# Performance work log

Measured on AMD Instinct MI355X. Metric: run time of the kernel, lower is better.

## Reference

```python
import jax, jax.numpy as jnp
import numpy as np

D = 1024      # in_features
E = 8         # num_experts
H = 4 * D     # expert hidden (expert_hidden_scale=4)
B, S = 2, 2048


def setup_inputs() -> dict:
    key = jax.random.key(0)
    k0, k1, k2, k3 = jax.random.split(key, 4)
    scale = 0.02
    x = jax.random.normal(k0, (B, S, D), dtype=jnp.float32)
    W_gate = (jax.random.normal(k1, (D, E), dtype=jnp.float32) * scale)      # gate.weight.T
    fc1_w = (jax.random.normal(k2, (E, 2 * H, D), dtype=jnp.float32) * scale)  # per-expert fc1 [out=2H, in=D]
    fc1_b = jnp.zeros((E, 2 * H), dtype=jnp.float32)
    fc2_w = (jax.random.normal(k3, (E, D, H), dtype=jnp.float32) * scale)      # per-expert fc2 [out=D, in=H]
    fc2_b = jnp.zeros((E, D), dtype=jnp.float32)
    return {"x": x, "W_gate": W_gate, "fc1_w": fc1_w, "fc1_b": fc1_b,
            "fc2_w": fc2_w, "fc2_b": fc2_b, "top_k": 2}


def reference(x, W_gate, fc1_w, fc1_b, fc2_w, fc2_b, top_k):
    # x: [B, S, D]. Dropout is identity (eval mode).
    b, s, d = x.shape
    e = W_gate.shape[1]
    xf = x.reshape(-1, d)                      # [N, D]
    n = xf.shape[0]

    gate_logits = xf @ W_gate                  # [N, E]
    top_vals, top_idx = jax.lax.top_k(gate_logits, top_k)          # [N, K]
    top_w = jax.nn.softmax(top_vals.astype(jnp.float32), axis=-1).astype(x.dtype)  # [N, K]

    # Every expert processes every token (matches the dense one-hot dispatch:
    # masked-out tokens get zero combine weight, so results are identical).
    h = jnp.einsum('nd,ehd->enh', xf, fc1_w) + fc1_b[:, None, :]   # [E, N, 2H]
    gate_h, val_h = jnp.split(h, 2, axis=-1)
    act = jax.nn.silu(gate_h) * val_h                               # [E, N, H]
    expert_out = jnp.einsum('enh,edh->end', act, fc2_w) + fc2_b[:, None, :]  # [E, N, D]

    onehot = jax.nn.one_hot(top_idx, e, dtype=x.dtype)             # [N, K, E]
    combine = jnp.einsum('nke,nk->en', onehot, top_w)              # [E, N]
    y = jnp.einsum('end,en->nd', expert_out, combine).reshape(b, s, d)

    frac_per_expert = onehot.sum(axis=(0, 1)) / n                  # [E]
    mean_prob = jax.nn.softmax(gate_logits, axis=-1).mean(axis=0)  # [E]
    aux_loss = e * jnp.sum(frac_per_expert * mean_prob)
    return y, aux_loss
```

## Files before the change

### kernel.cpp

```cpp
#include <hip/hip_runtime.h>
#include <hip/hip_bf16.h>
#include <cstdint>

#define NTOK 4096
#define DIM 1024
#define NEXP 8
#define HID 4096
#define TWO_H 8192
#define RCAP (NTOK*NEXP)
#define TOTROWS (NTOK*2)
#define ROWPAD (TOTROWS + 128)

typedef __attribute__((ext_vector_type(8))) short short8;
typedef __attribute__((ext_vector_type(4))) float f32x4;

__device__ __forceinline__ void async16(const void* g, void* l) {
    __builtin_amdgcn_global_load_lds(
        (const __attribute__((address_space(1))) unsigned int*)g,
        (__attribute__((address_space(3))) unsigned int*)l, 16, 0, 0);
}

__device__ __forceinline__ unsigned int packbf2(float a, float b) {
    union { __hip_bfloat16 h[2]; unsigned int u; } t;
    t.h[0] = __float2bfloat16(a); t.h[1] = __float2bfloat16(b);
    return t.u;
}

__global__ __launch_bounds__(256) void convert_kernel(const float* __restrict__ src,
                                                      __hip_bfloat16* __restrict__ dst, int n8) {
    int i = blockIdx.x * 256 + threadIdx.x;
    if (i >= n8) return;
    const float4* s = (const float4*)src + (size_t)i * 2;
    float4 a = s[0], b = s[1];
    uint4 o;
    o.x = packbf2(a.x, a.y); o.y = packbf2(a.z, a.w);
    o.z = packbf2(b.x, b.y); o.w = packbf2(b.z, b.w);
    ((uint4*)dst)[i] = o;
}

__global__ __launch_bounds__(256) void gate_kernel(
    const float* __restrict__ x, const float* __restrict__ Wg,
    float* __restrict__ p, float* __restrict__ topw,
    int* __restrict__ tok_list, int* __restrict__ klist, int* __restrict__ counts) {
    int n = blockIdx.x * 4 + (threadIdx.x >> 6);
    int lane = threadIdx.x & 63;
    const float* xr = x + (size_t)n * DIM;
    float acc[8];
#pragma unroll
    for (int e = 0; e < 8; e++) acc[e] = 0.f;
#pragma unroll
    for (int i = 0; i < 16; i++) {
        int d = i * 64 + lane;
        float xv = xr[d];
        const float4* wrow = (const float4*)(Wg + (size_t)d * 8);
        float4 w0 = wrow[0], w1 = wrow[1];
        acc[0] += xv * w0.x; acc[1] += xv * w0.y; acc[2] += xv * w0.z; acc[3] += xv * w0.w;
        acc[4] += xv * w1.x; acc[5] += xv * w1.y; acc[6] += xv * w1.z; acc[7] += xv * w1.w;
    }
#pragma unroll
    for (int m = 1; m < 64; m <<= 1) {
#pragma unroll
        for (int e = 0; e < 8; e++) acc[e] += __shfl_xor(acc[e], m, 64);
    }
    if (lane == 0) {
        int i0 = 0; float v0 = acc[0];
#pragma unroll
        for (int e = 1; e < 8; e++) if (acc[e] > v0) { v0 = acc[e]; i0 = e; }
        int i1 = -1; float v1 = -1e30f;
#pragma unroll
        for (int e = 0; e < 8; e++) if (e != i0 && acc[e] > v1) { v1 = acc[e]; i1 = e; }
        float ee = __expf(v1 - v0);
        float s = 1.f + ee;
        topw[2 * n] = 1.f / s;
        topw[2 * n + 1] = ee / s;
        float se = 0.f; float pe[8];
#pragma unroll
        for (int e = 0; e < 8; e++) { pe[e] = __expf(acc[e] - v0); se += pe[e]; }
        float inv = 1.f / se;
#pragma unroll
        for (int e = 0; e < 8; e++) p[(size_t)n * 8 + e] = pe[e] * inv;
        int p0 = atomicAdd(&counts[i0], 1);
        tok_list[i0 * NTOK + p0] = n; klist[i0 * NTOK + p0] = 0;
        int p1 = atomicAdd(&counts[i1], 1);
        tok_list[i1 * NTOK + p1] = n; klist[i1 * NTOK + p1] = 1;
    }
}

__global__ __launch_bounds__(256) void finalize_kernel(const float* __restrict__ p,
                                                       const int* __restrict__ counts,
                                                       int* __restrict__ offsets,
                                                       float* __restrict__ aux_out) {
    __shared__ float red[256];
    int t = threadIdx.x;
    float a = 0.f;
    for (int i = t; i < NTOK * NEXP; i += 256) a += p[i];
    red[t] = a;
    __syncthreads();
    if (t < 8) {
        float s = 0.f;
        for (int j = t; j < 256; j += 8) s += red[j];
        red[t] = s;
    }
    __syncthreads();
    if (t == 0) {
        int off = 0; float aux = 0.f;
        for (int e = 0; e < 8; e++) {
            offsets[e] = off;
            aux += ((float)counts[e] / (float)NTOK) * (red[e] / (float)NTOK);
            off += counts[e];
        }
        offsets[8] = off;
        aux_out[0] = 8.f * aux;
    }
}

__global__ __launch_bounds__(256) void pack_kernel(const float* __restrict__ x,
                                                   const int* __restrict__ tok_list,
                                                   const int* __restrict__ klist,
                                                   const int* __restrict__ counts,
                                                   const int* __restrict__ offsets,
                                                   __hip_bfloat16* __restrict__ xg,
                                                   int* __restrict__ prow) {
    int ci = blockIdx.x * 4 + (threadIdx.x >> 6);
    int lane = threadIdx.x & 63;
    int e = ci >> 12, pos = ci & (NTOK - 1);
    if (pos >= counts[e]) return;
    int tok = tok_list[ci];
    int r = offsets[e] + pos;
    const float4* src = (const float4*)(x + (size_t)tok * DIM);
    uint2* dst = (uint2*)(xg + (size_t)r * DIM);
#pragma unroll
    for (int i = 0; i < 4; i++) {
        int idx = i * 64 + lane;
        float4 v = src[idx];
        uint2 o; o.x = packbf2(v.x, v.y); o.y = packbf2(v.z, v.w);
        dst[idx] = o;
    }
    if (lane == 0) prow[tok * 2 + klist[ci]] = r;
}

__global__ __launch_bounds__(256, 2) void fc1_kernel(
    const __hip_bfloat16* __restrict__ xg, const __hip_bfloat16* __restrict__ w1b,
    const float* __restrict__ fc1b,
    __hip_bfloat16* __restrict__ act,
    const int* __restrict__ counts, const int* __restrict__ offsets) {
    int e = blockIdx.z;
    int cnt = counts[e];
    int rt = blockIdx.y;
    if (rt * 128 >= cnt) return;
    int ct = blockIdx.x;
    int row0 = offsets[e] + rt * 128;

    __shared__ __hip_bfloat16 As[128 * 64];
    __shared__ __hip_bfloat16 Bg[128 * 64];
    __shared__ __hip_bfloat16 Bv[128 * 64];

    int tid = threadIdx.x;
    int lane = tid & 63;
    int w = tid >> 6;
    int wr = w >> 1, wc = w & 1;
    int r = lane & 15, q = lane >> 4;

    const __hip_bfloat16* Abase = xg + (size_t)row0 * DIM;
    const __hip_bfloat16* Gbase = w1b + ((size_t)e * TWO_H + (size_t)ct * 128) * DIM;
    const __hip_bfloat16* Vbase = Gbase + (size_t)HID * DIM;

    size_t offA[4]; int ldsOff[4];
#pragma unroll
    for (int i = 0; i < 4; i++) {
        int c = w * 256 + i * 64 + lane;
        int m = c >> 3, kc = (c & 7) ^ (m & 7);
        offA[i] = (size_t)m * DIM + kc * 8;
        ldsOff[i] = (w * 256 + i * 64) * 8;
    }

    f32x4 accg[4][4], accv[4][4];
#pragma unroll
    for (int a = 0; a < 4; a++)
#pragma unroll
        for (int b = 0; b < 4; b++)
#pragma unroll
            for (int k = 0; k < 4; k++) { accg[a][b][k] = 0.f; accv[a][b][k] = 0.f; }

    for (int kb = 0; kb < DIM / 64; ++kb) {
        size_t ko = (size_t)kb * 64;
#pragma unroll
        for (int i = 0; i < 4; i++) {
            async16(Abase + offA[i] + ko, (void*)(As + ldsOff[i]));
            async16(Gbase + offA[i] + ko, (void*)(Bg + ldsOff[i]));
            async16(Vbase + offA[i] + ko, (void*)(Bv + ldsOff[i]));
        }
        __syncthreads();
#pragma unroll
        for (int ks = 0; ks < 2; ks++) {
            short8 af[4], bg[4], bv[4];
            int swz = ((ks * 4 + q) ^ (lane & 7)) * 8;
#pragma unroll
            for (int ti = 0; ti < 4; ti++) {
                int m = wr * 64 + ti * 16 + r;
                af[ti] = *(const short8*)(As + m * 64 + swz);
            }
#pragma unroll
            for (int tj = 0; tj < 4; tj++) {
                int n = wc * 64 + tj * 16 + r;
                bg[tj] = *(const short8*)(Bg + n * 64 + swz);
                bv[tj] = *(const short8*)(Bv + n * 64 + swz);
            }
#pragma unroll
            for (int ti = 0; ti < 4; ti++)
#pragma unroll
                for (int tj = 0; tj < 4; tj++) {
                    accg[ti][tj] = __builtin_amdgcn_mfma_f32_16x16x32_bf16(af[ti], bg[tj], accg[ti][tj], 0, 0, 0);
                    accv[ti][tj] = __builtin_amdgcn_mfma_f32_16x16x32_bf16(af[ti], bv[tj], accv[ti][tj], 0, 0, 0);
                }
        }
        __syncthreads();
    }

    const float* bgate = fc1b + (size_t)e * TWO_H + (size_t)ct * 128;
    const float* bval = bgate + HID;
#pragma unroll
    for (int ti = 0; ti < 4; ti++) {
#pragma unroll
        for (int tj = 0; tj < 4; tj++) {
            int coln = wc * 64 + tj * 16 + r;
            float bg_ = bgate[coln];
            float bv_ = bval[coln];
            f32x4 g = accg[ti][tj], v = accv[ti][tj];
#pragma unroll
            for (int rg = 0; rg < 4; rg++) {
                int lrow = wr * 64 + ti * 16 + q * 4 + rg;
                if (rt * 128 + lrow < cnt) {
                    float gv = g[rg] + bg_;
                    float vv = v[rg] + bv_;
                    float sil = gv / (1.f + __expf(-gv));
                    act[(size_t)(row0 + lrow) * HID + (size_t)ct * 128 + coln] = __float2bfloat16(sil * vv);
                }
            }
        }
    }
}

__global__ __launch_bounds__(256, 2) void fc2_kernel(
    const __hip_bfloat16* __restrict__ act, const __hip_bfloat16* __restrict__ w2b,
    const float* __restrict__ fc2b,
    float* __restrict__ eout,
    const int* __restrict__ counts, const int* __restrict__ offsets) {
    int e = blockIdx.z;
    int cnt = counts[e];
    int rt = blockIdx.y;
    if (rt * 128 >= cnt) return;
    int ct = blockIdx.x;
    int row0 = offsets[e] + rt * 128;

    __shared__ __hip_bfloat16 As[128 * 64];
    __shared__ __hip_bfloat16 Bs[128 * 64];

    int tid = threadIdx.x;
    int lane = tid & 63;
    int w = tid >> 6;
    int wr = w >> 1, wc = w & 1;
    int r = lane & 15, q = lane >> 4;

    const __hip_bfloat16* Abase = act + (size_t)row0 * HID;
    const __hip_bfloat16* Bbase = w2b + ((size_t)e * DIM + (size_t)ct * 128) * HID;

    size_t offA[4]; int ldsOff[4];
#pragma unroll
    for (int i = 0; i < 4; i++) {
        int c = w * 256 + i * 64 + lane;
        int m = c >> 3, kc = (c & 7) ^ (m & 7);
        offA[i] = (size_t)m * HID + kc * 8;
        ldsOff[i] = (w * 256 + i * 64) * 8;
    }

    f32x4 acc[4][4];
#pragma unroll
    for (int a = 0; a < 4; a++)
#pragma unroll
        for (int b = 0; b < 4; b++)
#pragma unroll
            for (int k = 0; k < 4; k++) acc[a][b][k] = 0.f;

    for (int kb = 0; kb < HID / 64; ++kb) {
        size_t ko = (size_t)kb * 64;
#pragma unroll
        for (int i = 0; i < 4; i++) {
            async16(Abase + offA[i] + ko, (void*)(As + ldsOff[i]));
            async16(Bbase + offA[i] + ko, (void*)(Bs + ldsOff[i]));
        }
        __syncthreads();
#pragma unroll
        for (int ks = 0; ks < 2; ks++) {
            short8 af[4], bf[4];
            int swz = ((ks * 4 + q) ^ (lane & 7)) * 8;
#pragma unroll
            for (int ti = 0; ti < 4; ti++) {
                int m = wr * 64 + ti * 16 + r;
                af[ti] = *(const short8*)(As + m * 64 + swz);
            }
#pragma unroll
            for (int tj = 0; tj < 4; tj++) {
                int n = wc * 64 + tj * 16 + r;
                bf[tj] = *(const short8*)(Bs + n * 64 + swz);
            }
#pragma unroll
            for (int ti = 0; ti < 4; ti++)
#pragma unroll
                for (int tj = 0; tj < 4; tj++)
                    acc[ti][tj] = __builtin_amdgcn_mfma_f32_16x16x32_bf16(af[ti], bf[tj], acc[ti][tj], 0, 0, 0);
        }
        __syncthreads();
    }

    const float* bias = fc2b + (size_t)e * DIM + (size_t)ct * 128;
#pragma unroll
    for (int ti = 0; ti < 4; ti++) {
#pragma unroll
        for (int tj = 0; tj < 4; tj++) {
            int coln = wc * 64 + tj * 16 + r;
            float b_ = bias[coln];
            f32x4 a = acc[ti][tj];
#pragma unroll
            for (int rg = 0; rg < 4; rg++) {
                int lrow = wr * 64 + ti * 16 + q * 4 + rg;
                if (rt * 128 + lrow < cnt)
                    eout[(size_t)(row0 + lrow) * DIM + (size_t)ct * 128 + coln] = a[rg] + b_;
            }
        }
    }
}

__global__ __launch_bounds__(256) void combine_kernel(const float* __restrict__ eout,
                                                      const int* __restrict__ prow,
                                                      const float* __restrict__ topw,
                                                      float* __restrict__ y) {
    int n = blockIdx.x;
    int t = threadIdx.x;
    int r0 = prow[2 * n], r1 = prow[2 * n + 1];
    float w0 = topw[2 * n], w1 = topw[2 * n + 1];
    const float4* a = (const float4*)(eout + (size_t)r0 * DIM);
    const float4* b = (const float4*)(eout + (size_t)r1 * DIM);
    float4 va = a[t], vb = b[t];
    float4 o;
    o.x = w0 * va.x + w1 * vb.x;
    o.y = w0 * va.y + w1 * vb.y;
    o.z = w0 * va.z + w1 * vb.z;
    o.w = w0 * va.w + w1 * vb.w;
    ((float4*)(y + (size_t)n * DIM))[t] = o;
}

extern "C" void kernel_launch(void* const* d_in, const int* in_sizes, int n_in,
                              void* d_out, int out_size, void* d_ws, size_t ws_size,
                              hipStream_t stream) {
    (void)in_sizes; (void)n_in; (void)out_size; (void)ws_size;
    const float* x = (const float*)d_in[0];
    const float* Wg = (const float*)d_in[1];
    const float* fc1w = (const float*)d_in[2];
    const float* fc1b = (const float*)d_in[3];
    const float* fc2w = (const float*)d_in[4];
    const float* fc2b = (const float*)d_in[5];
    float* out = (float*)d_out;

    char* wsp = (char*)d_ws;
    __hip_bfloat16* w1b = (__hip_bfloat16*)wsp;  wsp += (size_t)NEXP * TWO_H * DIM * 2;
    __hip_bfloat16* w2b = (__hip_bfloat16*)wsp;  wsp += (size_t)NEXP * DIM * HID * 2;
    __hip_bfloat16* xg = (__hip_bfloat16*)wsp;   wsp += (size_t)ROWPAD * DIM * 2;
    __hip_bfloat16* act = (__hip_bfloat16*)wsp;  wsp += (size_t)ROWPAD * HID * 2;
    float* eout = (float*)wsp;                   wsp += (size_t)TOTROWS * DIM * 4;
    float* p = (float*)wsp;                      wsp += (size_t)NTOK * NEXP * 4;
    float* topw = (float*)wsp;                   wsp += (size_t)NTOK * 2 * 4;
    int* tok_list = (int*)wsp;                   wsp += (size_t)RCAP * 4;
    int* klist = (int*)wsp;                      wsp += (size_t)RCAP * 4;
    int* prow = (int*)wsp;                       wsp += (size_t)NTOK * 2 * 4;
    int* counts = (int*)wsp;                     wsp += 64;
    int* offsets = (int*)wsp;                    wsp += 64;

    hipMemsetAsync(counts, 0, 8 * sizeof(int), stream);
    convert_kernel<<<32768, 256, 0, stream>>>(fc1w, w1b, (int)(NEXP * TWO_H * DIM / 8));
    convert_kernel<<<16384, 256, 0, stream>>>(fc2w, w2b, (int)(NEXP * DIM * HID / 8));
    gate_kernel<<<NTOK / 4, 256, 0, stream>>>(x, Wg, p, topw, tok_list, klist, counts);
    finalize_kernel<<<1, 256, 0, stream>>>(p, counts, offsets, out + (size_t)NTOK * DIM);
    pack_kernel<<<RCAP / 4, 256, 0, stream>>>(x, tok_list, klist, counts, offsets, xg, prow);
    fc1_kernel<<<dim3(HID / 128, 32, NEXP), 256, 0, stream>>>(xg, w1b, fc1b, act, counts, offsets);
    fc2_kernel<<<dim3(DIM / 128, 32, NEXP), 256, 0, stream>>>(act, w2b, fc2b, eout, counts, offsets);
    combine_kernel<<<NTOK, 256, 0, stream>>>(eout, prow, topw, out);
}
```

Baseline: 972.0 us.

## Fuse fp32-to-bf16 weight conversion into MoE GEMM B-operand loads

Removes the two standalone kernels that converted the full fc1 and fc2 weight tensors to bf16 in workspace. Each GEMM now reads fp32 weights straight from global memory into registers and packs them into bf16 MFMA fragments, skipping LDS for the B operand. Warp tiling changes so each wave covers all 128 rows and 32 columns, reusing the B fragments across 8 A fragments read from LDS. This drops a large conversion pass and its bf16 writes. In exchange, fp32 weights are re-read by every row tile at twice the bytes, and the global loads are not prefetched, so their latency is exposed before each barrier.

```diff
diff --git a/kernel.cpp b/kernel.cpp
--- a/kernel.cpp
+++ b/kernel.cpp
@@ -26,16 +26,11 @@
     return t.u;
 }
 
-__global__ __launch_bounds__(256) void convert_kernel(const float* __restrict__ src,
-                                                      __hip_bfloat16* __restrict__ dst, int n8) {
-    int i = blockIdx.x * 256 + threadIdx.x;
-    if (i >= n8) return;
-    const float4* s = (const float4*)src + (size_t)i * 2;
-    float4 a = s[0], b = s[1];
-    uint4 o;
-    o.x = packbf2(a.x, a.y); o.y = packbf2(a.z, a.w);
-    o.z = packbf2(b.x, b.y); o.w = packbf2(b.z, b.w);
-    ((uint4*)dst)[i] = o;
+__device__ __forceinline__ short8 cvtfrag(float4 f0, float4 f1) {
+    union { unsigned int u[4]; short8 s; } t;
+    t.u[0] = packbf2(f0.x, f0.y); t.u[1] = packbf2(f0.z, f0.w);
+    t.u[2] = packbf2(f1.x, f1.y); t.u[3] = packbf2(f1.z, f1.w);
+    return t.s;
 }
 
 __global__ __launch_bounds__(256) void gate_kernel(
@@ -140,7 +135,7 @@
 }
 
 __global__ __launch_bounds__(256, 2) void fc1_kernel(
-    const __hip_bfloat16* __restrict__ xg, const __hip_bfloat16* __restrict__ w1b,
+    const __hip_bfloat16* __restrict__ xg, const float* __restrict__ fc1w,
     const float* __restrict__ fc1b,
     __hip_bfloat16* __restrict__ act,
     const int* __restrict__ counts, const int* __restrict__ offsets) {
@@ -152,89 +147,87 @@
     int row0 = offsets[e] + rt * 128;
 
     __shared__ __hip_bfloat16 As[128 * 64];
-    __shared__ __hip_bfloat16 Bg[128 * 64];
-    __shared__ __hip_bfloat16 Bv[128 * 64];
 
     int tid = threadIdx.x;
     int lane = tid & 63;
     int w = tid >> 6;
-    int wr = w >> 1, wc = w & 1;
     int r = lane & 15, q = lane >> 4;
 
     const __hip_bfloat16* Abase = xg + (size_t)row0 * DIM;
-    const __hip_bfloat16* Gbase = w1b + ((size_t)e * TWO_H + (size_t)ct * 128) * DIM;
-    const __hip_bfloat16* Vbase = Gbase + (size_t)HID * DIM;
-
-    size_t offA[4]; int ldsOff[4];
+    const float* Gbase = fc1w + ((size_t)e * TWO_H + (size_t)ct * 128) * DIM;
+    const float* Vbase = Gbase + (size_t)HID * DIM;
+
+    size_t offA[4]; int ldsA[4];
 #pragma unroll
     for (int i = 0; i < 4; i++) {
         int c = w * 256 + i * 64 + lane;
         int m = c >> 3, kc = (c & 7) ^ (m & 7);
         offA[i] = (size_t)m * DIM + kc * 8;
-        ldsOff[i] = (w * 256 + i * 64) * 8;
-    }
-
-    f32x4 accg[4][4], accv[4][4];
-#pragma unroll
-    for (int a = 0; a < 4; a++)
-#pragma unroll
-        for (int b = 0; b < 4; b++)
+        ldsA[i] = (w * 256 + i * 64) * 8;
+    }
+
+    const float* g0 = Gbase + (size_t)(w * 32 + r) * DIM;
+    const float* g1 = Gbase + (size_t)(w * 32 + 16 + r) * DIM;
+    const float* v0 = Vbase + (size_t)(w * 32 + r) * DIM;
+    const float* v1 = Vbase + (size_t)(w * 32 + 16 + r) * DIM;
+
+    f32x4 accg[8][2], accv[8][2];
+#pragma unroll
+    for (int a = 0; a < 8; a++)
+#pragma unroll
+        for (int b = 0; b < 2; b++)
 #pragma unroll
             for (int k = 0; k < 4; k++) { accg[a][b][k] = 0.f; accv[a][b][k] = 0.f; }
 
     for (int kb = 0; kb < DIM / 64; ++kb) {
-        size_t ko = (size_t)kb * 64;
-#pragma unroll
-        for (int i = 0; i < 4; i++) {
-            async16(Abase + offA[i] + ko, (void*)(As + ldsOff[i]));
-            async16(Gbase + offA[i] + ko, (void*)(Bg + ldsOff[i]));
-            async16(Vbase + offA[i] + ko, (void*)(Bv + ldsOff[i]));
+        int ko = kb * 64;
+#pragma unroll
+        for (int i = 0; i < 4; i++) async16(Abase + offA[i] + ko, (void*)(As + ldsA[i]));
+
+        short8 bg[2][2], bv[2][2];
+#pragma unroll
+        for (int ks = 0; ks < 2; ks++) {
+            int kk = ko + ks * 32 + q * 8;
+            const float4* pg0 = (const float4*)(g0 + kk);
+            const float4* pg1 = (const float4*)(g1 + kk);
+            const float4* pv0 = (const float4*)(v0 + kk);
+            const float4* pv1 = (const float4*)(v1 + kk);
+            bg[ks][0] = cvtfrag(pg0[0], pg0[1]);
+            bg[ks][1] = cvtfrag(pg1[0], pg1[1]);
+            bv[ks][0] = cvtfrag(pv0[0], pv0[1]);
+            bv[ks][1] = cvtfrag(pv1[0], pv1[1]);
         }
         __syncthreads();
 #pragma unroll
         for (int ks = 0; ks < 2; ks++) {
-            short8 af[4], bg[4], bv[4];
             int swz = ((ks * 4 + q) ^ (lane & 7)) * 8;
 #pragma unroll
-            for (int ti = 0; ti < 4; ti++) {
-                int m = wr * 64 + ti * 16 + r;
-                af[ti] = *(const short8*)(As + m * 64 + swz);
+            for (int ti = 0; ti < 8; ti++) {
+                short8 af = *(const short8*)(As + (ti * 16 + r) * 64 + swz);
+                accg[ti][0] = __builtin_amdgcn_mfma_f32_16x16x32_bf16(af, bg[ks][0], accg[ti][0], 0, 0, 0);
+                accg[ti][1] = __builtin_amdgcn_mfma_f32_16x16x32_bf16(af, bg[ks][1], accg[ti][1], 0, 0, 0);
+                accv[ti][0] = __builtin_amdgcn_mfma_f32_16x16x32_bf16(af, bv[ks][0], accv[ti][0], 0, 0, 0);
+                accv[ti][1] = __builtin_amdgcn_mfma_f32_16x16x32_bf16(af, bv[ks][1], accv[ti][1], 0, 0, 0);
             }
-#pragma unroll
-            for (int tj = 0; tj < 4; tj++) {
-                int n = wc * 64 + tj * 16 + r;
-                bg[tj] = *(const short8*)(Bg + n * 64 + swz);
-                bv[tj] = *(const short8*)(Bv + n * 64 + swz);
-            }
-#pragma unroll
-            for (int ti = 0; ti < 4; ti++)
-#pragma unroll
-                for (int tj = 0; tj < 4; tj++) {
-                    accg[ti][tj] = __builtin_amdgcn_mfma_f32_16x16x32_bf16(af[ti], bg[tj], accg[ti][tj], 0, 0, 0);
-                    accv[ti][tj] = __builtin_amdgcn_mfma_f32_16x16x32_bf16(af[ti], bv[tj], accv[ti][tj], 0, 0, 0);
-                }
         }
         __syncthreads();
     }
 
-    const float* bgate = fc1b + (size_t)e * TWO_H + (size_t)ct * 128;
-    const float* bval = bgate + HID;
-#pragma unroll
-    for (int ti = 0; ti < 4; ti++) {
-#pragma unroll
-        for (int tj = 0; tj < 4; tj++) {
-            int coln = wc * 64 + tj * 16 + r;
-            float bg_ = bgate[coln];
-            float bv_ = bval[coln];
-            f32x4 g = accg[ti][tj], v = accv[ti][tj];
+#pragma unroll
+    for (int tj = 0; tj < 2; tj++) {
+        int cg = ct * 128 + w * 32 + tj * 16 + r;
+        float bg_ = fc1b[(size_t)e * TWO_H + cg];
+        float bv_ = fc1b[(size_t)e * TWO_H + HID + cg];
+#pragma unroll
+        for (int ti = 0; ti < 8; ti++) {
 #pragma unroll
             for (int rg = 0; rg < 4; rg++) {
-                int lrow = wr * 64 + ti * 16 + q * 4 + rg;
+                int lrow = ti * 16 + q * 4 + rg;
                 if (rt * 128 + lrow < cnt) {
-                    float gv = g[rg] + bg_;
-                    float vv = v[rg] + bv_;
+                    float gv = accg[ti][tj][rg] + bg_;
+                    float vv = accv[ti][tj][rg] + bv_;
                     float sil = gv / (1.f + __expf(-gv));
-                    act[(size_t)(row0 + lrow) * HID + (size_t)ct * 128 + coln] = __float2bfloat16(sil * vv);
+                    act[(size_t)(row0 + lrow) * HID + cg] = __float2bfloat16(sil * vv);
                 }
             }
         }
@@ -242,7 +235,7 @@
 }
 
 __global__ __launch_bounds__(256, 2) void fc2_kernel(
-    const __hip_bfloat16* __restrict__ act, const __hip_bfloat16* __restrict__ w2b,
+    const __hip_bfloat16* __restrict__ act, const float* __restrict__ fc2w,
     const float* __restrict__ fc2b,
     float* __restrict__ eout,
     const int* __restrict__ counts, const int* __restrict__ offsets) {
@@ -254,78 +247,74 @@
     int row0 = offsets[e] + rt * 128;
 
     __shared__ __hip_bfloat16 As[128 * 64];
-    __shared__ __hip_bfloat16 Bs[128 * 64];
 
     int tid = threadIdx.x;
     int lane = tid & 63;
     int w = tid >> 6;
-    int wr = w >> 1, wc = w & 1;
     int r = lane & 15, q = lane >> 4;
 
     const __hip_bfloat16* Abase = act + (size_t)row0 * HID;
-    const __hip_bfloat16* Bbase = w2b + ((size_t)e * DIM + (size_t)ct * 128) * HID;
-
-    size_t offA[4]; int ldsOff[4];
+    const float* Bbase = fc2w + ((size_t)e * DIM + (size_t)ct * 128) * HID;
+
+    size_t offA[4]; int ldsA[4];
 #pragma unroll
     for (int i = 0; i < 4; i++) {
         int c = w * 256 + i * 64 + lane;
         int m = c >> 3, kc = (c & 7) ^ (m & 7);
         offA[i] = (size_t)m * HID + kc * 8;
-        ldsOff[i] = (w * 256 + i * 64) * 8;
-    }
-
-    f32x4 acc[4][4];
-#pragma unroll
-    for (int a = 0; a < 4; a++)
-#pragma unroll
-        for (int b = 0; b < 4; b++)
+        ldsA[i] = (w * 256 + i * 64) * 8;
+    }
+
+    const float* b0 = Bbase + (size_t)(w * 32 + r) * HID;
+    const float* b1 = Bbase + (size_t)(w * 32 + 16 + r) * HID;
+
+    f32x4 acc[8][2];
+#pragma unroll
+    for (int a = 0; a < 8; a++)
+#pragma unroll
+        for (int b = 0; b < 2; b++)
 #pragma unroll
             for (int k = 0; k < 4; k++) acc[a][b][k] = 0.f;
 
     for (int kb = 0; kb < HID / 64; ++kb) {
-        size_t ko = (size_t)kb * 64;
-#pragma unroll
-        for (int i = 0; i < 4; i++) {
-            async16(Abase + offA[i] + ko, (void*)(As + ldsOff[i]));
-            async16(Bbase + offA[i] + ko, (void*)(Bs + ldsOff[i]));
+        int ko = kb * 64;
+#pragma unroll
+        for (int i = 0; i < 4; i++) async16(Abase + offA[i] + ko, (void*)(As + ldsA[i]));
+
+        short8 bb[2][2];
+#pragma unroll
+        for (int ks = 0; ks < 2; ks++) {
+            int kk = ko + ks * 32 + q * 8;
+            const float4* p0 = (const float4*)(b0 + kk);
+            const float4* p1 = (const float4*)(b1 + kk);
+            bb[ks][0] = cvtfrag(p0[0], p0[1]);
+            bb[ks][1] = cvtfrag(p1[0], p1[1]);
         }
         __syncthreads();
 #pragma unroll
         for (int ks = 0; ks < 2; ks++) {
-            short8 af[4], bf[4];
             int swz = ((ks * 4 + q) ^ (lane & 7)) * 8;
 #pragma unroll
-            for (int ti = 0; ti < 4; ti++) {
-                int m = wr * 64 + ti * 16 + r;
-                af[ti] = *(const short8*)(As + m * 64 + swz);
+            for (int ti = 0; ti < 8; ti++) {
+                short8 af = *(const short8*)(As + (ti * 16 + r) * 64 + swz);
+                acc[ti][0] = __builtin_amdgcn_mfma_f32_16x16x32_bf16(af, bb[ks][0], acc[ti][0], 0, 0, 0);
+                acc[ti][1] = __builtin_amdgcn_mfma_f32_16x16x32_bf16(af, bb[ks][1], acc[ti][1], 0, 0, 0);
             }
-#pragma unroll
-            for (int tj = 0; tj < 4; tj++) {
-                int n = wc * 64 + tj * 16 + r;
-                bf[tj] = *(const short8*)(Bs + n * 64 + swz);
-            }
-#pragma unroll
-            for (int ti = 0; ti < 4; ti++)
-#pragma unroll
-                for (int tj = 0; tj < 4; tj++)
-                    acc[ti][tj] = __builtin_amdgcn_mfma_f32_16x16x32_bf16(af[ti], bf[tj], acc[ti][tj], 0, 0, 0);
         }
         __syncthreads();
     }
 
-    const float* bias = fc2b + (size_t)e * DIM + (size_t)ct * 128;
-#pragma unroll
-    for (int ti = 0; ti < 4; ti++) {
-#pragma unroll
-        for (int tj = 0; tj < 4; tj++) {
-            int coln = wc * 64 + tj * 16 + r;
-            float b_ = bias[coln];
-            f32x4 a = acc[ti][tj];
+#pragma unroll
+    for (int tj = 0; tj < 2; tj++) {
+        int col = ct * 128 + w * 32 + tj * 16 + r;
+        float b_ = fc2b[(size_t)e * DIM + col];
+#pragma unroll
+        for (int ti = 0; ti < 8; ti++) {
 #pragma unroll
             for (int rg = 0; rg < 4; rg++) {
-                int lrow = wr * 64 + ti * 16 + q * 4 + rg;
+                int lrow = ti * 16 + q * 4 + rg;
                 if (rt * 128 + lrow < cnt)
-                    eout[(size_t)(row0 + lrow) * DIM + (size_t)ct * 128 + coln] = a[rg] + b_;
+                    eout[(size_t)(row0 + lrow) * DIM + col] = acc[ti][tj][rg] + b_;
             }
         }
     }
@@ -363,8 +352,6 @@
     float* out = (float*)d_out;
 
     char* wsp = (char*)d_ws;
-    __hip_bfloat16* w1b = (__hip_bfloat16*)wsp;  wsp += (size_t)NEXP * TWO_H * DIM * 2;
-    __hip_bfloat16* w2b = (__hip_bfloat16*)wsp;  wsp += (size_t)NEXP * DIM * HID * 2;
     __hip_bfloat16* xg = (__hip_bfloat16*)wsp;   wsp += (size_t)ROWPAD * DIM * 2;
     __hip_bfloat16* act = (__hip_bfloat16*)wsp;  wsp += (size_t)ROWPAD * HID * 2;
     float* eout = (float*)wsp;                   wsp += (size_t)TOTROWS * DIM * 4;
@@ -377,12 +364,10 @@
     int* offsets = (int*)wsp;                    wsp += 64;
 
     hipMemsetAsync(counts, 0, 8 * sizeof(int), stream);
-    convert_kernel<<<32768, 256, 0, stream>>>(fc1w, w1b, (int)(NEXP * TWO_H * DIM / 8));
-    convert_kernel<<<16384, 256, 0, stream>>>(fc2w, w2b, (int)(NEXP * DIM * HID / 8));
     gate_kernel<<<NTOK / 4, 256, 0, stream>>>(x, Wg, p, topw, tok_list, klist, counts);
     finalize_kernel<<<1, 256, 0, stream>>>(p, counts, offsets, out + (size_t)NTOK * DIM);
     pack_kernel<<<RCAP / 4, 256, 0, stream>>>(x, tok_list, klist, counts, offsets, xg, prow);
-    fc1_kernel<<<dim3(HID / 128, 32, NEXP), 256, 0, stream>>>(xg, w1b, fc1b, act, counts, offsets);
-    fc2_kernel<<<dim3(DIM / 128, 32, NEXP), 256, 0, stream>>>(act, w2b, fc2b, eout, counts, offsets);
+    fc1_kernel<<<dim3(HID / 128, 32, NEXP), 256, 0, stream>>>(xg, fc1w, fc1b, act, counts, offsets);
+    fc2_kernel<<<dim3(DIM / 128, 32, NEXP), 256, 0, stream>>>(act, fc2w, fc2b, eout, counts, offsets);
     combine_kernel<<<NTOK, 256, 0, stream>>>(eout, prow, topw, out);
 }
```

After: 1.200 ms. 1.23x slower.

## Deterministic routing scan, fused combine into fc2 via atomics, merged convert launches

Applied to the files above, without the earlier changes.

Replaces atomic-counter token routing with per-block histograms plus a single-block prefix scan, so pack runs one wave per token and writes both expert rows. The combine kernel and the fp32 expert-output buffer are removed: fc2 now scales its results by the gate weight and atomically adds them into a zeroed output. The two weight conversion launches become one, and the memset moves from the counters to the output. This cuts launches and the expert-output round-trip through memory, at the cost of float atomics in the fc2 epilogue and a serial scan over 1024 blocks.

```diff
diff --git a/kernel.cpp b/kernel.cpp
--- a/kernel.cpp
+++ b/kernel.cpp
@@ -7,9 +7,9 @@
 #define NEXP 8
 #define HID 4096
 #define TWO_H 8192
-#define RCAP (NTOK*NEXP)
 #define TOTROWS (NTOK*2)
 #define ROWPAD (TOTROWS + 128)
+#define GBLK (NTOK/4)
 
 typedef __attribute__((ext_vector_type(8))) short short8;
 typedef __attribute__((ext_vector_type(4))) float f32x4;
@@ -26,24 +26,32 @@
     return t.u;
 }
 
-__global__ __launch_bounds__(256) void convert_kernel(const float* __restrict__ src,
-                                                      __hip_bfloat16* __restrict__ dst, int n8) {
+__global__ __launch_bounds__(256) void convert_kernel(const float* __restrict__ fc1w,
+                                                      const float* __restrict__ fc2w,
+                                                      __hip_bfloat16* __restrict__ w1b,
+                                                      __hip_bfloat16* __restrict__ w2b) {
+    const int n1 = NEXP * TWO_H * DIM / 8;
     int i = blockIdx.x * 256 + threadIdx.x;
-    if (i >= n8) return;
-    const float4* s = (const float4*)src + (size_t)i * 2;
-    float4 a = s[0], b = s[1];
+    const float* s; __hip_bfloat16* d; int j;
+    if (i < n1) { s = fc1w; d = w1b; j = i; }
+    else        { s = fc2w; d = w2b; j = i - n1; }
+    const float4* sp = (const float4*)s + (size_t)j * 2;
+    float4 a = sp[0], b = sp[1];
     uint4 o;
     o.x = packbf2(a.x, a.y); o.y = packbf2(a.z, a.w);
     o.z = packbf2(b.x, b.y); o.w = packbf2(b.z, b.w);
-    ((uint4*)dst)[i] = o;
+    ((uint4*)d)[j] = o;
 }
 
 __global__ __launch_bounds__(256) void gate_kernel(
     const float* __restrict__ x, const float* __restrict__ Wg,
-    float* __restrict__ p, float* __restrict__ topw,
-    int* __restrict__ tok_list, int* __restrict__ klist, int* __restrict__ counts) {
-    int n = blockIdx.x * 4 + (threadIdx.x >> 6);
+    float* __restrict__ topw, int* __restrict__ einfo,
+    int* __restrict__ ghist, float* __restrict__ gpsum) {
+    __shared__ float probs[4][8];
+    __shared__ int epair[4][2];
+    int wv = threadIdx.x >> 6;
     int lane = threadIdx.x & 63;
+    int n = blockIdx.x * 4 + wv;
     const float* xr = x + (size_t)n * DIM;
     float acc[8];
 #pragma unroll
@@ -78,65 +86,102 @@
         for (int e = 0; e < 8; e++) { pe[e] = __expf(acc[e] - v0); se += pe[e]; }
         float inv = 1.f / se;
 #pragma unroll
-        for (int e = 0; e < 8; e++) p[(size_t)n * 8 + e] = pe[e] * inv;
-        int p0 = atomicAdd(&counts[i0], 1);
-        tok_list[i0 * NTOK + p0] = n; klist[i0 * NTOK + p0] = 0;
-        int p1 = atomicAdd(&counts[i1], 1);
-        tok_list[i1 * NTOK + p1] = n; klist[i1 * NTOK + p1] = 1;
-    }
-}
-
-__global__ __launch_bounds__(256) void finalize_kernel(const float* __restrict__ p,
-                                                       const int* __restrict__ counts,
-                                                       int* __restrict__ offsets,
-                                                       float* __restrict__ aux_out) {
-    __shared__ float red[256];
+        for (int e = 0; e < 8; e++) probs[wv][e] = pe[e] * inv;
+        epair[wv][0] = i0; epair[wv][1] = i1;
+    }
+    __syncthreads();
     int t = threadIdx.x;
-    float a = 0.f;
-    for (int i = t; i < NTOK * NEXP; i += 256) a += p[i];
-    red[t] = a;
+    if (t < 8) {
+        gpsum[blockIdx.x * 8 + t] = probs[0][t] + probs[1][t] + probs[2][t] + probs[3][t];
+    }
+    if (t == 0) {
+        int h[8];
+#pragma unroll
+        for (int e = 0; e < 8; e++) h[e] = 0;
+        int inf[4];
+#pragma unroll
+        for (int tt = 0; tt < 4; tt++) {
+            int e0 = epair[tt][0], e1 = epair[tt][1];
+            int r0 = h[e0]++, r1 = h[e1]++;
+            inf[tt] = e0 | (e1 << 4) | (r0 << 8) | (r1 << 12);
+        }
+#pragma unroll
+        for (int tt = 0; tt < 4; tt++) einfo[blockIdx.x * 4 + tt] = inf[tt];
+#pragma unroll
+        for (int e = 0; e < 8; e++) ghist[blockIdx.x * 8 + e] = h[e];
+    }
+}
+
+__global__ __launch_bounds__(256) void scan_kernel(
+    const int* __restrict__ ghist, const float* __restrict__ gpsum,
+    int* __restrict__ gbase, int* __restrict__ counts, int* __restrict__ offsets,
+    float* __restrict__ aux_out) {
+    __shared__ int hist[GBLK * 8];
+    __shared__ float psum[GBLK * 8];
+    __shared__ int counts_s[8];
+    __shared__ int offs[9];
+    __shared__ float psum_e[8];
+    int t = threadIdx.x;
+    for (int i = t; i < GBLK * 8; i += 256) { hist[i] = ghist[i]; psum[i] = gpsum[i]; }
     __syncthreads();
     if (t < 8) {
-        float s = 0.f;
-        for (int j = t; j < 256; j += 8) s += red[j];
-        red[t] = s;
+        int run = 0;
+        float ps = 0.f;
+        for (int b = 0; b < GBLK; b++) {
+            int v = hist[b * 8 + t];
+            hist[b * 8 + t] = run;
+            run += v;
+            ps += psum[b * 8 + t];
+        }
+        counts_s[t] = run;
+        psum_e[t] = ps;
     }
     __syncthreads();
     if (t == 0) {
         int off = 0; float aux = 0.f;
         for (int e = 0; e < 8; e++) {
+            offs[e] = off;
+            counts[e] = counts_s[e];
             offsets[e] = off;
-            aux += ((float)counts[e] / (float)NTOK) * (red[e] / (float)NTOK);
-            off += counts[e];
-        }
-        offsets[8] = off;
+            aux += ((float)counts_s[e] / (float)NTOK) * (psum_e[e] / (float)NTOK);
+            off += counts_s[e];
+        }
+        offs[8] = off; offsets[8] = off;
         aux_out[0] = 8.f * aux;
     }
+    __syncthreads();
+    for (int i = t; i < GBLK * 8; i += 256) gbase[i] = hist[i] + offs[i & 7];
 }
 
 __global__ __launch_bounds__(256) void pack_kernel(const float* __restrict__ x,
-                                                   const int* __restrict__ tok_list,
-                                                   const int* __restrict__ klist,
-                                                   const int* __restrict__ counts,
-                                                   const int* __restrict__ offsets,
+                                                   const int* __restrict__ einfo,
+                                                   const int* __restrict__ gbase,
                                                    __hip_bfloat16* __restrict__ xg,
-                                                   int* __restrict__ prow) {
-    int ci = blockIdx.x * 4 + (threadIdx.x >> 6);
+                                                   int* __restrict__ rowinfo) {
+    int wv = threadIdx.x >> 6;
     int lane = threadIdx.x & 63;
-    int e = ci >> 12, pos = ci & (NTOK - 1);
-    if (pos >= counts[e]) return;
-    int tok = tok_list[ci];
-    int r = offsets[e] + pos;
-    const float4* src = (const float4*)(x + (size_t)tok * DIM);
-    uint2* dst = (uint2*)(xg + (size_t)r * DIM);
+    int n = blockIdx.x * 4 + wv;
+    int info = einfo[n];
+    int e0 = info & 15, e1 = (info >> 4) & 15;
+    int r0 = (info >> 8) & 15, r1 = (info >> 12) & 15;
+    int blk = blockIdx.x;
+    int row0 = gbase[blk * 8 + e0] + r0;
+    int row1 = gbase[blk * 8 + e1] + r1;
+    const float4* src = (const float4*)(x + (size_t)n * DIM);
+    uint2* d0 = (uint2*)(xg + (size_t)row0 * DIM);
+    uint2* d1 = (uint2*)(xg + (size_t)row1 * DIM);
 #pragma unroll
     for (int i = 0; i < 4; i++) {
         int idx = i * 64 + lane;
         float4 v = src[idx];
         uint2 o; o.x = packbf2(v.x, v.y); o.y = packbf2(v.z, v.w);
-        dst[idx] = o;
-    }
-    if (lane == 0) prow[tok * 2 + klist[ci]] = r;
+        d0[idx] = o;
+        d1[idx] = o;
+    }
+    if (lane == 0) {
+        rowinfo[row0] = 2 * n;
+        rowinfo[row1] = 2 * n + 1;
+    }
 }
 
 __global__ __launch_bounds__(256, 2) void fc1_kernel(
@@ -244,7 +289,8 @@
 __global__ __launch_bounds__(256, 2) void fc2_kernel(
     const __hip_bfloat16* __restrict__ act, const __hip_bfloat16* __restrict__ w2b,
     const float* __restrict__ fc2b,
-    float* __restrict__ eout,
+    const int* __restrict__ rowinfo, const float* __restrict__ topw,
+    float* __restrict__ out,
     const int* __restrict__ counts, const int* __restrict__ offsets) {
     int e = blockIdx.z;
     int cnt = counts[e];
@@ -316,6 +362,16 @@
     const float* bias = fc2b + (size_t)e * DIM + (size_t)ct * 128;
 #pragma unroll
     for (int ti = 0; ti < 4; ti++) {
+        int inf[4]; float wgt[4]; int ok[4];
+#pragma unroll
+        for (int rg = 0; rg < 4; rg++) {
+            int lrow = wr * 64 + ti * 16 + q * 4 + rg;
+            ok[rg] = (rt * 128 + lrow < cnt);
+            if (ok[rg]) {
+                inf[rg] = rowinfo[row0 + lrow];
+                wgt[rg] = topw[inf[rg]];
+            }
+        }
 #pragma unroll
         for (int tj = 0; tj < 4; tj++) {
             int coln = wc * 64 + tj * 16 + r;
@@ -323,31 +379,14 @@
             f32x4 a = acc[ti][tj];
 #pragma unroll
             for (int rg = 0; rg < 4; rg++) {
-                int lrow = wr * 64 + ti * 16 + q * 4 + rg;
-                if (rt * 128 + lrow < cnt)
-                    eout[(size_t)(row0 + lrow) * DIM + (size_t)ct * 128 + coln] = a[rg] + b_;
-            }
-        }
-    }
-}
-
-__global__ __launch_bounds__(256) void combine_kernel(const float* __restrict__ eout,
-                                                      const int* __restrict__ prow,
-                                                      const float* __restrict__ topw,
-                                                      float* __restrict__ y) {
-    int n = blockIdx.x;
-    int t = threadIdx.x;
-    int r0 = prow[2 * n], r1 = prow[2 * n + 1];
-    float w0 = topw[2 * n], w1 = topw[2 * n + 1];
-    const float4* a = (const float4*)(eout + (size_t)r0 * DIM);
-    const float4* b = (const float4*)(eout + (size_t)r1 * DIM);
-    float4 va = a[t], vb = b[t];
-    float4 o;
-    o.x = w0 * va.x + w1 * vb.x;
-    o.y = w0 * va.y + w1 * vb.y;
-    o.z = w0 * va.z + w1 * vb.z;
-    o.w = w0 * va.w + w1 * vb.w;
-    ((float4*)(y + (size_t)n * DIM))[t] = o;
+                if (ok[rg]) {
+                    int tok = inf[rg] >> 1;
+                    atomicAdd(&out[(size_t)tok * DIM + (size_t)ct * 128 + coln],
+                              wgt[rg] * (a[rg] + b_));
+                }
+            }
+        }
+    }
 }
 
 extern "C" void kernel_launch(void* const* d_in, const int* in_sizes, int n_in,
@@ -367,22 +406,22 @@
     __hip_bfloat16* w2b = (__hip_bfloat16*)wsp;  wsp += (size_t)NEXP * DIM * HID * 2;
     __hip_bfloat16* xg = (__hip_bfloat16*)wsp;   wsp += (size_t)ROWPAD * DIM * 2;
     __hip_bfloat16* act = (__hip_bfloat16*)wsp;  wsp += (size_t)ROWPAD * HID * 2;
-    float* eout = (float*)wsp;                   wsp += (size_t)TOTROWS * DIM * 4;
-    float* p = (float*)wsp;                      wsp += (size_t)NTOK * NEXP * 4;
     float* topw = (float*)wsp;                   wsp += (size_t)NTOK * 2 * 4;
-    int* tok_list = (int*)wsp;                   wsp += (size_t)RCAP * 4;
-    int* klist = (int*)wsp;                      wsp += (size_t)RCAP * 4;
-    int* prow = (int*)wsp;                       wsp += (size_t)NTOK * 2 * 4;
+    int* einfo = (int*)wsp;                      wsp += (size_t)NTOK * 4;
+    int* ghist = (int*)wsp;                      wsp += (size_t)GBLK * 8 * 4;
+    float* gpsum = (float*)wsp;                  wsp += (size_t)GBLK * 8 * 4;
+    int* gbase = (int*)wsp;                      wsp += (size_t)GBLK * 8 * 4;
+    int* rowinfo = (int*)wsp;                    wsp += (size_t)TOTROWS * 4;
     int* counts = (int*)wsp;                     wsp += 64;
     int* offsets = (int*)wsp;                    wsp += 64;
 
-    hipMemsetAsync(counts, 0, 8 * sizeof(int), stream);
-    convert_kernel<<<32768, 256, 0, stream>>>(fc1w, w1b, (int)(NEXP * TWO_H * DIM / 8));
-    convert_kernel<<<16384, 256, 0, stream>>>(fc2w, w2b, (int)(NEXP * DIM * HID / 8));
-    gate_kernel<<<NTOK / 4, 256, 0, stream>>>(x, Wg, p, topw, tok_list, klist, counts);
-    finalize_kernel<<<1, 256, 0, stream>>>(p, counts, offsets, out + (size_t)NTOK * DIM);
-    pack_kernel<<<RCAP / 4, 256, 0, stream>>>(x, tok_list, klist, counts, offsets, xg, prow);
+    hipMemsetAsync(out, 0, (size_t)NTOK * DIM * sizeof(float), stream);
+    convert_kernel<<<49152, 256, 0, stream>>>(fc1w, fc2w, w1b, w2b);
+    gate_kernel<<<GBLK, 256, 0, stream>>>(x, Wg, topw, einfo, ghist, gpsum);
+    scan_kernel<<<1, 256, 0, stream>>>(ghist, gpsum, gbase, counts, offsets,
+                                       out + (size_t)NTOK * DIM);
+    pack_kernel<<<GBLK, 256, 0, stream>>>(x, einfo, gbase, xg, rowinfo);
     fc1_kernel<<<dim3(HID / 128, 32, NEXP), 256, 0, stream>>>(xg, w1b, fc1b, act, counts, offsets);
-    fc2_kernel<<<dim3(DIM / 128, 32, NEXP), 256, 0, stream>>>(act, w2b, fc2b, eout, counts, offsets);
-    combine_kernel<<<NTOK, 256, 0, stream>>>(eout, prow, topw, out);
-}
+    fc2_kernel<<<dim3(DIM / 128, 32, NEXP), 256, 0, stream>>>(act, w2b, fc2b, rowinfo, topw,
+                                                              out, counts, offsets);
+}
```

New measurement: 885.6 us. 1.1x faster.
